# Kernel tuning notes

Measured on AMD Instinct MI355X. Metric: run time of the kernel, lower is better.

Reference implementation:

```python
import jax, jax.numpy as jnp
import numpy as np

B, N, E = 32, 1024, 512   # docs, word-nodes per doc, hyperedges per doc
V = 50001                 # n_node + 1 (padding idx 0)
D = 300                   # initialFeatureSize == n_hid
H = 300                   # hiddenSize (output of gat2)
NEG = -9e15


def _leaky(v, alpha):
    return jnp.where(v > 0, v, alpha * v)


def _hypergat_layer(x, adj, w, w2, w3, a, a2, wc, alpha, concat):
    # x: [B,N,Fin], adj: [B,E,N] 0/1 incidence. Eval mode: dropout = identity.
    Fo = w2.shape[1]
    x4 = x @ w2                                   # [B,N,Fo]
    if w is not None:                             # transfer=True branch
        x = x @ w                                 # [B,N,Fo]
    mask = adj > 0                                # [B,E,N]
    # edge attention: score per node, constant word-context query
    s1 = _leaky(wc @ a[:Fo, 0] + x4 @ a[Fo:, 0], alpha)          # [B,N]
    att_edge = jax.nn.softmax(jnp.where(mask, s1[:, None, :], NEG), axis=2)  # [B,E,N]
    edge = att_edge @ x                           # [B,E,Fo] hyperedge features
    edge4 = edge @ w3                             # [B,E,Fo]
    # node attention: score(node n, edge e) = leaky(x4[n]@a2_top + edge4[e]@a2_bot)
    sc = _leaky((x4 @ a2[:Fo, 0])[:, None, :] + (edge4 @ a2[Fo:, 0])[:, :, None], alpha)  # [B,E,N]
    att_node = jax.nn.softmax(jnp.where(mask, sc, NEG).transpose(0, 2, 1), axis=2)        # [B,N,E]
    node = att_node @ edge                        # [B,N,Fo]
    return jax.nn.elu(node) if concat else node


def setup_inputs() -> dict:
    key = jax.random.key(0)
    ks = jax.random.split(key, 16)
    stdv = 1.0 / np.sqrt(H)  # DocumentGraph.reset_parameters uniform_(-stdv, stdv) on all params
    u = lambda k, shape: jax.random.uniform(k, shape, jnp.float32, -stdv, stdv)
    return dict(
        inputs=jax.random.randint(ks[0], (B, N), 0, V),
        HT=(jax.random.uniform(ks[1], (B, E, N)) < 0.10).astype(jnp.int32),
        emb=u(ks[2], (V, D)),
        w2_1=u(ks[3], (D, D)), w3_1=u(ks[4], (D, D)),
        a_1=u(ks[5], (2 * D, 1)), a2_1=u(ks[6], (2 * D, 1)), wc_1=u(ks[7], (D,)),
        w_2=u(ks[8], (D, H)), w2_2=u(ks[9], (D, H)), w3_2=u(ks[10], (H, H)),
        a_2=u(ks[11], (2 * H, 1)), a2_2=u(ks[12], (2 * H, 1)), wc_2=u(ks[13], (H,)),
    )


def reference(inputs, HT, emb, w2_1, w3_1, a_1, a2_1, wc_1,
              w_2, w2_2, w3_2, a_2, a2_2, wc_2):
    x = emb[inputs]                                # [B,N,D] embedding lookup
    # gat1: transfer=False, concat=True, alpha=0.1
    x = _hypergat_layer(x, HT, None, w2_1, w3_1, a_1, a2_1, wc_1, 0.1, True)
    # gat2: transfer=True, bias=False, concat=False, alpha=0.2
    x = _hypergat_layer(x, HT, w_2, w2_2, w3_2, a_2, a2_2, wc_2, 0.2, False)
    return x
```

## Files before the change

### kernel.cpp

```cpp
#include <hip/hip_runtime.h>
#include <hip/hip_bf16.h>

#define CB 32
#define CN 1024
#define CE 512
#define CD 300
#define EP 320
#define UCAP 320

__global__ void k_embed(const int* __restrict__ idx, const float* __restrict__ emb,
                        float* __restrict__ X) {
    int gid = blockIdx.x * blockDim.x + threadIdx.x;
    const int total = CB * CN * 75;
    if (gid >= total) return;
    int r = gid / 75, c = gid % 75;
    int e = idx[r];
    reinterpret_cast<float4*>(X)[(size_t)r * 75 + c] =
        reinterpret_cast<const float4*>(emb)[(size_t)e * 75 + c];
}

__global__ void k_transpose(const int* __restrict__ HT, unsigned char* __restrict__ HTt) {
    __shared__ int tile[32][33];
    int b = blockIdx.z;
    int e0 = blockIdx.x * 32, n0 = blockIdx.y * 32;
    int tx = threadIdx.x, ty = threadIdx.y;
    for (int i = ty; i < 32; i += 8)
        tile[i][tx] = HT[((size_t)b * CE + e0 + i) * CN + n0 + tx];
    __syncthreads();
    for (int i = ty; i < 32; i += 8)
        HTt[((size_t)b * CN + n0 + i) * CE + e0 + tx] = (unsigned char)(tile[tx][i] > 0 ? 1 : 0);
}

__global__ void k_ebits(const int* __restrict__ HT, unsigned long long* __restrict__ ebits) {
    int gw = (blockIdx.x * blockDim.x + threadIdx.x) >> 6;
    int lane = threadIdx.x & 63;
    const int* hrow = HT + (size_t)gw * CN;
#pragma unroll
    for (int c = 0; c < 16; ++c) {
        unsigned long long bal = __ballot(hrow[(c << 6) + lane] != 0);
        if (lane == 0) ebits[(size_t)gw * 16 + c] = bal;
    }
}

__global__ void k_nbits(const unsigned char* __restrict__ HTt, unsigned long long* __restrict__ nbits) {
    int row = (blockIdx.x * blockDim.x + threadIdx.x) >> 6;
    int lane = threadIdx.x & 63;
    const unsigned char* hrow = HTt + (size_t)row * CE;
#pragma unroll
    for (int c = 0; c < 8; ++c) {
        unsigned long long bal = __ballot(hrow[(c << 6) + lane] != 0);
        if (lane == 0) nbits[(size_t)row * 8 + c] = bal;
    }
}

__global__ void k_prep(const float* __restrict__ w2_1, const float* __restrict__ w3_1,
                       const float* __restrict__ a_1, const float* __restrict__ a2_1,
                       const float* __restrict__ w2_2, const float* __restrict__ w3_2,
                       const float* __restrict__ a_2, const float* __restrict__ a2_2,
                       float* __restrict__ vecs) {
    int which = blockIdx.x;
    int t = threadIdx.x;
    if (t >= CD) return;
    const float* W; const float* v;
    switch (which) {
        case 0:  W = w2_1; v = a_1 + CD;  break;
        case 1:  W = w2_1; v = a2_1;      break;
        case 2:  W = w3_1; v = a2_1 + CD; break;
        case 3:  W = w2_2; v = a_2 + CD;  break;
        case 4:  W = w2_2; v = a2_2;      break;
        default: W = w3_2; v = a2_2 + CD; break;
    }
    float s = 0.f;
    for (int j = 0; j < CD; ++j) s += W[(size_t)t * CD + j] * v[j];
    vecs[which * CD + t] = s;
}

__global__ __launch_bounds__(256) void k_gemm300(const float* __restrict__ A,
                                                 const float* __restrict__ W,
                                                 float* __restrict__ C, int M,
                                                 int lda, int ldc) {
    __shared__ float As[64][20];
    __shared__ float Ws[16][68];
    int tid = threadIdx.x;
    int n0 = blockIdx.x * 64, m0 = blockIdx.y * 64;
    int tx = tid & 15, ty = tid >> 4;
    int la_r = tid >> 2, la_c = (tid & 3) << 2;
    int lw_r = tid >> 4, lw_c = (tid & 15) << 2;
    float acc[4][4] = {};
    for (int k0 = 0; k0 < CD; k0 += 16) {
        {
            int kc = k0 + la_c;
            const float* Ap = A + (size_t)(m0 + la_r) * lda + kc;
            float4 av;
            if (kc + 3 < CD) av = *reinterpret_cast<const float4*>(Ap);
            else {
                av.x = kc     < CD ? Ap[0] : 0.f;
                av.y = kc + 1 < CD ? Ap[1] : 0.f;
                av.z = kc + 2 < CD ? Ap[2] : 0.f;
                av.w = 0.f;
            }
            *reinterpret_cast<float4*>(&As[la_r][la_c]) = av;
        }
        {
            int kr = k0 + lw_r;
            float4 wv = {0.f, 0.f, 0.f, 0.f};
            if (kr < CD) {
                const float* Wp = W + (size_t)kr * CD + n0 + lw_c;
                if (n0 + lw_c + 3 < CD) wv = *reinterpret_cast<const float4*>(Wp);
                else {
                    if (n0 + lw_c     < CD) wv.x = Wp[0];
                    if (n0 + lw_c + 1 < CD) wv.y = Wp[1];
                    if (n0 + lw_c + 2 < CD) wv.z = Wp[2];
                }
            }
            *reinterpret_cast<float4*>(&Ws[lw_r][lw_c]) = wv;
        }
        __syncthreads();
#pragma unroll
        for (int k = 0; k < 16; ++k) {
            float av[4];
#pragma unroll
            for (int i = 0; i < 4; ++i) av[i] = As[ty * 4 + i][k];
            float4 bv = *reinterpret_cast<const float4*>(&Ws[k][tx * 4]);
            float bb[4] = {bv.x, bv.y, bv.z, bv.w};
#pragma unroll
            for (int i = 0; i < 4; ++i)
#pragma unroll
                for (int j = 0; j < 4; ++j) acc[i][j] += av[i] * bb[j];
        }
        __syncthreads();
    }
    for (int i = 0; i < 4; ++i) {
        int m = m0 + ty * 4 + i;
        int n = n0 + tx * 4;
        float* Cp = C + (size_t)m * ldc + n;
        if (n + 3 < CD) {
            float4 v = {acc[i][0], acc[i][1], acc[i][2], acc[i][3]};
            *reinterpret_cast<float4*>(Cp) = v;
        } else {
            for (int j = 0; j < 4; ++j) if (n + j < CD) Cp[j] = acc[i][j];
        }
    }
}

__global__ void k_score(const float* __restrict__ X, const float* __restrict__ av,
                        const float* __restrict__ pv, const float* __restrict__ wc,
                        const float* __restrict__ a_orig,
                        float alpha, float* __restrict__ s1, float* __restrict__ p, int M) {
    int gw = (blockIdx.x * blockDim.x + threadIdx.x) >> 6;
    int lane = threadIdx.x & 63;
    if (gw >= M) return;
    const float* row = X + (size_t)gw * CD;
    float d1 = 0.f, d2 = 0.f, dc = 0.f;
    for (int d = lane; d < CD; d += 64) {
        float x = row[d];
        d1 += x * av[d];
        d2 += x * pv[d];
        dc += wc[d] * a_orig[d];
    }
    for (int o = 32; o; o >>= 1) {
        d1 += __shfl_down(d1, o);
        d2 += __shfl_down(d2, o);
        dc += __shfl_down(dc, o);
    }
    if (lane == 0) {
        float v = dc + d1;
        s1[gw] = v > 0.f ? v : alpha * v;
        p[gw] = d2;
    }
}

__global__ __launch_bounds__(1024) void k_bmax(const float* __restrict__ s1,
                                               float* __restrict__ e1) {
    __shared__ float red[16];
    int b = blockIdx.x, t = threadIdx.x;
    float v = s1[b * CN + t];
    float m = v;
    for (int o = 32; o; o >>= 1) m = fmaxf(m, __shfl_xor(m, o));
    if ((t & 63) == 0) red[t >> 6] = m;
    __syncthreads();
    if (t == 0) {
        float mm = red[0];
        for (int i = 1; i < 16; ++i) mm = fmaxf(mm, red[i]);
        red[0] = mm;
    }
    __syncthreads();
    e1[b * CN + t] = __expf(v - red[0]);
}

__global__ __launch_bounds__(256) void k_edge_agg(const unsigned long long* __restrict__ ebits,
        const float* __restrict__ e1, const float* __restrict__ Xs,
        const float* __restrict__ qvec, float* __restrict__ edge, float* __restrict__ q) {
    int i = blockIdx.x;
    int r = i & 7, t = i >> 3;
    int b = (t >> 7) * 8 + r;
    int j = t & 127;
    int gw = b * CE + (j << 2) + (threadIdx.x >> 6);
    int lane = threadIdx.x & 63;
    const unsigned long long* eb = ebits + (size_t)gw * 16;
    const float* e1b = e1 + b * CN;
    const float* Xb = Xs + (size_t)b * CN * CD;
    float acc[5] = {};
    float den = 0.f;
    bool tail = lane < (CD - 256);
    int any = 0;
#pragma unroll
    for (int c = 0; c < 16; ++c) {
        int n0 = c << 6;
        float wv = e1b[n0 + lane];
        unsigned long long bal = eb[c];
        any |= (bal != 0ull);
        while (bal) {
            int jj = (int)__ffsll(bal) - 1;
            bal &= bal - 1ull;
            float w = __shfl(wv, jj);
            const float* row = Xb + (size_t)(n0 + jj) * CD;
            den += w;
            acc[0] += w * row[lane];
            acc[1] += w * row[lane + 64];
            acc[2] += w * row[lane + 128];
            acc[3] += w * row[lane + 192];
            if (tail) acc[4] += w * row[lane + 256];
        }
    }
    float inv = any ? 1.f / den : 0.f;
    float* erow = edge + (size_t)gw * EP;
    float o0 = acc[0] * inv, o1 = acc[1] * inv, o2 = acc[2] * inv, o3 = acc[3] * inv;
    float o4 = tail ? acc[4] * inv : 0.f;
    erow[lane]       = o0;
    erow[lane + 64]  = o1;
    erow[lane + 128] = o2;
    erow[lane + 192] = o3;
    erow[lane + 256] = o4;
    float d2 = o0 * qvec[lane];
    d2 += o1 * qvec[lane + 64];
    d2 += o2 * qvec[lane + 128];
    d2 += o3 * qvec[lane + 192];
    if (tail) d2 += o4 * qvec[lane + 256];
    for (int o = 32; o; o >>= 1) d2 += __shfl_down(d2, o);
    if (lane == 0) q[gw] = d2;
}

#define ACC16(vv, ww) do { \
    acc[0][0] += (ww).x * (vv).x; acc[0][1] += (ww).x * (vv).y; \
    acc[0][2] += (ww).x * (vv).z; acc[0][3] += (ww).x * (vv).w; \
    acc[1][0] += (ww).y * (vv).x; acc[1][1] += (ww).y * (vv).y; \
    acc[1][2] += (ww).y * (vv).z; acc[1][3] += (ww).y * (vv).w; \
    acc[2][0] += (ww).z * (vv).x; acc[2][1] += (ww).z * (vv).y; \
    acc[2][2] += (ww).z * (vv).z; acc[2][3] += (ww).z * (vv).w; \
    acc[3][0] += (ww).w * (vv).x; acc[3][1] += (ww).w * (vv).y; \
    acc[3][2] += (ww).w * (vv).z; acc[3][3] += (ww).w * (vv).w; \
} while (0)

__global__ __launch_bounds__(320, 8) void k_node_attn(const unsigned long long* __restrict__ nbits,
        const float* __restrict__ p, const float* __restrict__ q,
        const float* __restrict__ edge, float alpha, int do_elu, float* __restrict__ out) {
    __shared__ float4 wsc[4][UCAP];
    __shared__ __align__(8) unsigned short ul[4][UCAP];
    __shared__ int ucnt_s[4], flag_s[4];
    __shared__ float gpn[16], gmx[16], gsc[16];
    __shared__ int gct[16];
    int i0 = blockIdx.x;
    int rr = i0 & 7, tt = i0 >> 3;
    int b = (tt >> 6) * 8 + rr;
    int n0 = (tt & 63) << 4;
    int tid = threadIdx.x, wv = tid >> 6, lane = tid & 63;
    const float* qb = q + b * CE;

    if (wv < 4) {
        float pn[4]; const unsigned long long* nb[4];
#pragma unroll
        for (int k = 0; k < 4; ++k) {
            int n = n0 + 4 * wv + k;
            pn[k] = p[b * CN + n];
            nb[k] = nbits + ((size_t)b * CN + n) * 8;
        }
        float sc[4][8];
        int cnt[4] = {0, 0, 0, 0};
        float mx[4] = {-3.4e38f, -3.4e38f, -3.4e38f, -3.4e38f};
        int ubits = 0;
#pragma unroll
        for (int j = 0; j < 8; ++j) {
            int e = lane + (j << 6);
            float qe = qb[e];
            int many = 0;
#pragma unroll
            for (int k = 0; k < 4; ++k) {
                int m = (int)((nb[k][j] >> lane) & 1ull);
                float v = pn[k] + qe;
                v = v > 0.f ? v : alpha * v;
                v = m ? v : -3.0e38f;
                cnt[k] += m; many |= m;
                mx[k] = fmaxf(mx[k], v);
                sc[k][j] = v;
            }
            ubits |= (many ? 1 : 0) << j;
        }
#pragma unroll
        for (int k = 0; k < 4; ++k) {
            for (int o = 32; o; o >>= 1) {
                mx[k] = fmaxf(mx[k], __shfl_xor(mx[k], o));
                cnt[k] += __shfl_xor(cnt[k], o);
            }
        }
        float scale[4];
#pragma unroll
        for (int k = 0; k < 4; ++k) {
            float s = 0.f;
#pragma unroll
            for (int j = 0; j < 8; ++j) { float w8 = __expf(sc[k][j] - mx[k]); sc[k][j] = w8; s += w8; }
            for (int o = 32; o; o >>= 1) s += __shfl_xor(s, o);
            scale[k] = cnt[k] > 0 ? 1.f / s : 1.f;
        }
        int base = 0;
        unsigned long long lmask = (1ull << lane) - 1ull;
#pragma unroll
        for (int j = 0; j < 8; ++j) {
            unsigned long long bal = __ballot((ubits >> j) & 1);
            if ((ubits >> j) & 1) {
                int off = base + (int)__popcll(bal & lmask);
                if (off < UCAP) {
                    ul[wv][off] = (unsigned short)(lane + (j << 6));
                    wsc[wv][off] = make_float4(sc[0][j] * scale[0], sc[1][j] * scale[1],
                                               sc[2][j] * scale[2], sc[3][j] * scale[3]);
                }
            }
            base += (int)__popcll(bal);
        }
        if (lane == 0) {
            ucnt_s[wv] = base < UCAP ? base : UCAP;
            flag_s[wv] = (cnt[0] == 0) | (cnt[1] == 0) | (cnt[2] == 0) | (cnt[3] == 0) |
                         (base > UCAP);
            gpn[wv*4+0]=pn[0]; gmx[wv*4+0]=mx[0]; gsc[wv*4+0]=scale[0]; gct[wv*4+0]=cnt[0];
            gpn[wv*4+1]=pn[1]; gmx[wv*4+1]=mx[1]; gsc[wv*4+1]=scale[1]; gct[wv*4+1]=cnt[1];
            gpn[wv*4+2]=pn[2]; gmx[wv*4+2]=mx[2]; gsc[wv*4+2]=scale[2]; gct[wv*4+2]=cnt[2];
            gpn[wv*4+3]=pn[3]; gmx[wv*4+3]=mx[3]; gsc[wv*4+3]=scale[3]; gct[wv*4+3]=cnt[3];
        }
    }
    __syncthreads();

    int grp = tid / 80;
    int j4 = tid - grp * 80;
    const float4* eb4 = reinterpret_cast<const float4*>(edge + (size_t)b * CE * EP) + j4;
    int cnt = ucnt_s[grp], bad = flag_s[grp];
    float acc[4][4] = {};
    if (!bad) {
        int i = 0;
        for (; i + 4 <= cnt; i += 4) {
            ushort4 uu = *reinterpret_cast<const ushort4*>(&ul[grp][i]);
            float4 w0 = wsc[grp][i],     w1 = wsc[grp][i + 1];
            float4 w2 = wsc[grp][i + 2], w3 = wsc[grp][i + 3];
            float4 v0 = eb4[(size_t)uu.x * 80], v1 = eb4[(size_t)uu.y * 80];
            float4 v2 = eb4[(size_t)uu.z * 80], v3 = eb4[(size_t)uu.w * 80];
            ACC16(v0, w0); ACC16(v1, w1); ACC16(v2, w2); ACC16(v3, w3);
        }
        for (; i < cnt; ++i) {
            int e = ul[grp][i];
            float4 v = eb4[(size_t)e * 80];
            float4 w = wsc[grp][i];
            ACC16(v, w);
        }
    } else {
        float pnk[4], mxk[4], sck[4]; int ctk[4];
        const unsigned long long* nbr[4];
#pragma unroll
        for (int k = 0; k < 4; ++k) {
            pnk[k] = gpn[grp*4+k]; mxk[k] = gmx[grp*4+k]; sck[k] = gsc[grp*4+k]; ctk[k] = gct[grp*4+k];
            nbr[k] = nbits + ((size_t)b * CN + n0 + grp * 4 + k) * 8;
        }
        for (int e = 0; e < CE; ++e) {
            float4 v = eb4[(size_t)e * 80];
            float qe = qb[e];
#pragma unroll
            for (int k = 0; k < 4; ++k) {
                int m = (int)((nbr[k][e >> 6] >> (e & 63)) & 1ull);
                float vv = pnk[k] + qe; vv = vv > 0.f ? vv : alpha * vv;
                float w = ctk[k] == 0 ? (1.f / CE) : (m ? __expf(vv - mxk[k]) * sck[k] : 0.f);
                acc[k][0] += w * v.x; acc[k][1] += w * v.y; acc[k][2] += w * v.z; acc[k][3] += w * v.w;
            }
        }
    }
    if (j4 < 75) {
#pragma unroll
        for (int ni = 0; ni < 4; ++ni) {
            float4 o = {acc[ni][0], acc[ni][1], acc[ni][2], acc[ni][3]};
            if (do_elu) {
                o.x = o.x > 0.f ? o.x : expm1f(o.x);
                o.y = o.y > 0.f ? o.y : expm1f(o.y);
                o.z = o.z > 0.f ? o.z : expm1f(o.z);
                o.w = o.w > 0.f ? o.w : expm1f(o.w);
            }
            *reinterpret_cast<float4*>(out + ((size_t)b * CN + n0 + grp * 4 + ni) * CD + j4 * 4) = o;
        }
    }
}

extern "C" void kernel_launch(void* const* d_in, const int* in_sizes, int n_in,
                              void* d_out, int out_size, void* d_ws, size_t ws_size,
                              hipStream_t stream) {
    const int*   inputs = (const int*)d_in[0];
    const int*   HT     = (const int*)d_in[1];
    const float* emb    = (const float*)d_in[2];
    const float* w2_1   = (const float*)d_in[3];
    const float* w3_1   = (const float*)d_in[4];
    const float* a_1    = (const float*)d_in[5];
    const float* a2_1   = (const float*)d_in[6];
    const float* wc_1   = (const float*)d_in[7];
    const float* w_2    = (const float*)d_in[8];
    const float* w2_2   = (const float*)d_in[9];
    const float* w3_2   = (const float*)d_in[10];
    const float* a_2    = (const float*)d_in[11];
    const float* a2_2   = (const float*)d_in[12];
    const float* wc_2   = (const float*)d_in[13];

    char* ws = (char*)d_ws;
    float* big0                   = (float*)(ws);
    float* big1                   = (float*)(ws + 39321600);
    float* edge                   = (float*)(ws + 78643200);
    unsigned char* HTt            = (unsigned char*)(ws + 99614720);
    unsigned long long* ebits     = (unsigned long long*)(ws + 116391936);
    unsigned long long* nbits     = (unsigned long long*)(ws + 118489088);
    float* s1                     = (float*)(ws + 120586240);
    float* p                      = (float*)(ws + 120717312);
    float* e1                     = (float*)(ws + 120848384);
    float* qv                     = (float*)(ws + 120979456);
    float* vecs                   = (float*)(ws + 121044992);

    k_embed<<<9600, 256, 0, stream>>>(inputs, emb, big0);
    k_transpose<<<dim3(16, 32, 32), dim3(32, 8), 0, stream>>>(HT, HTt);
    k_ebits<<<4096, 256, 0, stream>>>(HT, ebits);
    k_nbits<<<8192, 256, 0, stream>>>(HTt, nbits);
    k_prep<<<6, 320, 0, stream>>>(w2_1, w3_1, a_1, a2_1, w2_2, w3_2, a_2, a2_2, vecs);

    k_score<<<CB * CN / 4, 256, 0, stream>>>(big0, vecs, vecs + CD, wc_1, a_1, 0.1f, s1, p, CB * CN);
    k_bmax<<<CB, 1024, 0, stream>>>(s1, e1);
    k_edge_agg<<<4096, 256, 0, stream>>>(ebits, e1, big0, vecs + 2 * CD, edge, qv);
    k_node_attn<<<2048, 320, 0, stream>>>(nbits, p, qv, edge, 0.1f, 1, big0);

    k_score<<<CB * CN / 4, 256, 0, stream>>>(big0, vecs + 3 * CD, vecs + 4 * CD, wc_2, a_2, 0.2f, s1, p, CB * CN);
    k_gemm300<<<dim3(5, 512), 256, 0, stream>>>(big0, w_2, big1, CB * CN, CD, CD);
    k_bmax<<<CB, 1024, 0, stream>>>(s1, e1);
    k_edge_agg<<<4096, 256, 0, stream>>>(ebits, e1, big1, vecs + 5 * CD, edge, qv);
    k_node_attn<<<2048, 320, 0, stream>>>(nbits, p, qv, edge, 0.2f, 0, (float*)d_out);
}
```

Measured before the change: 675.1 us.

## Build node bitmasks by bit-transposing edge bitmasks; vectorize edge aggregation loads

```diff
diff --git a/kernel.cpp b/kernel.cpp
--- a/kernel.cpp
+++ b/kernel.cpp
@@ -19,18 +19,6 @@
         reinterpret_cast<const float4*>(emb)[(size_t)e * 75 + c];
 }
 
-__global__ void k_transpose(const int* __restrict__ HT, unsigned char* __restrict__ HTt) {
-    __shared__ int tile[32][33];
-    int b = blockIdx.z;
-    int e0 = blockIdx.x * 32, n0 = blockIdx.y * 32;
-    int tx = threadIdx.x, ty = threadIdx.y;
-    for (int i = ty; i < 32; i += 8)
-        tile[i][tx] = HT[((size_t)b * CE + e0 + i) * CN + n0 + tx];
-    __syncthreads();
-    for (int i = ty; i < 32; i += 8)
-        HTt[((size_t)b * CN + n0 + i) * CE + e0 + tx] = (unsigned char)(tile[tx][i] > 0 ? 1 : 0);
-}
-
 __global__ void k_ebits(const int* __restrict__ HT, unsigned long long* __restrict__ ebits) {
     int gw = (blockIdx.x * blockDim.x + threadIdx.x) >> 6;
     int lane = threadIdx.x & 63;
@@ -42,15 +30,18 @@
     }
 }
 
-__global__ void k_nbits(const unsigned char* __restrict__ HTt, unsigned long long* __restrict__ nbits) {
-    int row = (blockIdx.x * blockDim.x + threadIdx.x) >> 6;
-    int lane = threadIdx.x & 63;
-    const unsigned char* hrow = HTt + (size_t)row * CE;
-#pragma unroll
-    for (int c = 0; c < 8; ++c) {
-        unsigned long long bal = __ballot(hrow[(c << 6) + lane] != 0);
-        if (lane == 0) nbits[(size_t)row * 8 + c] = bal;
-    }
+__global__ __launch_bounds__(512) void k_bitT(const unsigned long long* __restrict__ ebits,
+        unsigned long long* __restrict__ nbits) {
+    __shared__ unsigned long long w[8][64];
+    int b = blockIdx.x >> 4, nc = blockIdx.x & 15;
+    int tid = threadIdx.x, ec = tid >> 6, lane = tid & 63;
+    w[ec][lane] = ebits[((size_t)b * CE + (ec << 6) + lane) * 16 + nc];
+    __syncthreads();
+    unsigned long long out = 0;
+#pragma unroll
+    for (int j = 0; j < 64; ++j)
+        out |= ((w[ec][j] >> lane) & 1ull) << j;
+    nbits[((size_t)b * CN + (nc << 6) + lane) * 8 + ec] = out;
 }
 
 __global__ void k_prep(const float* __restrict__ w2_1, const float* __restrict__ w3_1,
@@ -191,18 +182,15 @@
 __global__ __launch_bounds__(256) void k_edge_agg(const unsigned long long* __restrict__ ebits,
         const float* __restrict__ e1, const float* __restrict__ Xs,
         const float* __restrict__ qvec, float* __restrict__ edge, float* __restrict__ q) {
-    int i = blockIdx.x;
-    int r = i & 7, t = i >> 3;
-    int b = (t >> 7) * 8 + r;
-    int j = t & 127;
-    int gw = b * CE + (j << 2) + (threadIdx.x >> 6);
+    int gw = (blockIdx.x * blockDim.x + threadIdx.x) >> 6;
     int lane = threadIdx.x & 63;
+    int b = gw >> 9;
     const unsigned long long* eb = ebits + (size_t)gw * 16;
     const float* e1b = e1 + b * CN;
-    const float* Xb = Xs + (size_t)b * CN * CD;
-    float acc[5] = {};
+    const float4* Xb4 = reinterpret_cast<const float4*>(Xs + (size_t)b * CN * CD);
+    float4 a0 = {0.f, 0.f, 0.f, 0.f}, a1 = {0.f, 0.f, 0.f, 0.f};
     float den = 0.f;
-    bool tail = lane < (CD - 256);
+    bool tail = lane < 11;
     int any = 0;
 #pragma unroll
     for (int c = 0; c < 16; ++c) {
@@ -211,32 +199,50 @@
         unsigned long long bal = eb[c];
         any |= (bal != 0ull);
         while (bal) {
-            int jj = (int)__ffsll(bal) - 1;
-            bal &= bal - 1ull;
-            float w = __shfl(wv, jj);
-            const float* row = Xb + (size_t)(n0 + jj) * CD;
-            den += w;
-            acc[0] += w * row[lane];
-            acc[1] += w * row[lane + 64];
-            acc[2] += w * row[lane + 128];
-            acc[3] += w * row[lane + 192];
-            if (tail) acc[4] += w * row[lane + 256];
+            int j0 = (int)__ffsll(bal) - 1; bal &= bal - 1ull;
+            float w0 = __shfl(wv, j0);
+            const float4* r0 = Xb4 + (size_t)(n0 + j0) * 75;
+            if (bal) {
+                int j1 = (int)__ffsll(bal) - 1; bal &= bal - 1ull;
+                float w1 = __shfl(wv, j1);
+                const float4* r1 = Xb4 + (size_t)(n0 + j1) * 75;
+                float4 v0a = r0[lane];
+                float4 v1a = r1[lane];
+                float4 v0b, v1b;
+                if (tail) { v0b = r0[64 + lane]; v1b = r1[64 + lane]; }
+                den += w0; den += w1;
+                a0.x += w0 * v0a.x; a0.y += w0 * v0a.y; a0.z += w0 * v0a.z; a0.w += w0 * v0a.w;
+                a0.x += w1 * v1a.x; a0.y += w1 * v1a.y; a0.z += w1 * v1a.z; a0.w += w1 * v1a.w;
+                if (tail) {
+                    a1.x += w0 * v0b.x; a1.y += w0 * v0b.y; a1.z += w0 * v0b.z; a1.w += w0 * v0b.w;
+                    a1.x += w1 * v1b.x; a1.y += w1 * v1b.y; a1.z += w1 * v1b.z; a1.w += w1 * v1b.w;
+                }
+            } else {
+                float4 v0a = r0[lane];
+                float4 v0b;
+                if (tail) v0b = r0[64 + lane];
+                den += w0;
+                a0.x += w0 * v0a.x; a0.y += w0 * v0a.y; a0.z += w0 * v0a.z; a0.w += w0 * v0a.w;
+                if (tail) {
+                    a1.x += w0 * v0b.x; a1.y += w0 * v0b.y; a1.z += w0 * v0b.z; a1.w += w0 * v0b.w;
+                }
+            }
         }
     }
     float inv = any ? 1.f / den : 0.f;
-    float* erow = edge + (size_t)gw * EP;
-    float o0 = acc[0] * inv, o1 = acc[1] * inv, o2 = acc[2] * inv, o3 = acc[3] * inv;
-    float o4 = tail ? acc[4] * inv : 0.f;
-    erow[lane]       = o0;
-    erow[lane + 64]  = o1;
-    erow[lane + 128] = o2;
-    erow[lane + 192] = o3;
-    erow[lane + 256] = o4;
-    float d2 = o0 * qvec[lane];
-    d2 += o1 * qvec[lane + 64];
-    d2 += o2 * qvec[lane + 128];
-    d2 += o3 * qvec[lane + 192];
-    if (tail) d2 += o4 * qvec[lane + 256];
+    float4 o0 = {a0.x * inv, a0.y * inv, a0.z * inv, a0.w * inv};
+    float4 o1 = {a1.x * inv, a1.y * inv, a1.z * inv, a1.w * inv};
+    float4* er4 = reinterpret_cast<float4*>(edge + (size_t)gw * EP);
+    er4[lane] = o0;
+    if (tail) er4[64 + lane] = o1;
+    else if (lane < 16) er4[64 + lane] = make_float4(0.f, 0.f, 0.f, 0.f);
+    const float4* qv4 = reinterpret_cast<const float4*>(qvec);
+    float4 qa = qv4[lane];
+    float d2 = o0.x * qa.x + o0.y * qa.y + o0.z * qa.z + o0.w * qa.w;
+    if (tail) {
+        float4 qb2 = qv4[64 + lane];
+        d2 += o1.x * qb2.x + o1.y * qb2.y + o1.z * qb2.z + o1.w * qb2.w;
+    }
     for (int o = 32; o; o >>= 1) d2 += __shfl_down(d2, o);
     if (lane == 0) q[gw] = d2;
 }
@@ -260,10 +266,8 @@
     __shared__ int ucnt_s[4], flag_s[4];
     __shared__ float gpn[16], gmx[16], gsc[16];
     __shared__ int gct[16];
-    int i0 = blockIdx.x;
-    int rr = i0 & 7, tt = i0 >> 3;
-    int b = (tt >> 6) * 8 + rr;
-    int n0 = (tt & 63) << 4;
+    int blk = blockIdx.x;
+    int b = blk >> 6, n0 = (blk & 63) << 4;
     int tid = threadIdx.x, wv = tid >> 6, lane = tid & 63;
     const float* qb = q + b * CE;
 
@@ -414,22 +418,20 @@
     const float* wc_2   = (const float*)d_in[13];
 
     char* ws = (char*)d_ws;
-    float* big0                   = (float*)(ws);
-    float* big1                   = (float*)(ws + 39321600);
-    float* edge                   = (float*)(ws + 78643200);
-    unsigned char* HTt            = (unsigned char*)(ws + 99614720);
-    unsigned long long* ebits     = (unsigned long long*)(ws + 116391936);
-    unsigned long long* nbits     = (unsigned long long*)(ws + 118489088);
-    float* s1                     = (float*)(ws + 120586240);
-    float* p                      = (float*)(ws + 120717312);
-    float* e1                     = (float*)(ws + 120848384);
-    float* qv                     = (float*)(ws + 120979456);
-    float* vecs                   = (float*)(ws + 121044992);
+    float* big0               = (float*)(ws);
+    float* big1               = (float*)(ws + 39321600);
+    float* edge               = (float*)(ws + 78643200);
+    unsigned long long* ebits = (unsigned long long*)(ws + 99614720);
+    unsigned long long* nbits = (unsigned long long*)(ws + 101711872);
+    float* s1                 = (float*)(ws + 103809024);
+    float* p                  = (float*)(ws + 103940096);
+    float* e1                 = (float*)(ws + 104071168);
+    float* qv                 = (float*)(ws + 104202240);
+    float* vecs               = (float*)(ws + 104267776);
 
     k_embed<<<9600, 256, 0, stream>>>(inputs, emb, big0);
-    k_transpose<<<dim3(16, 32, 32), dim3(32, 8), 0, stream>>>(HT, HTt);
     k_ebits<<<4096, 256, 0, stream>>>(HT, ebits);
-    k_nbits<<<8192, 256, 0, stream>>>(HTt, nbits);
+    k_bitT<<<512, 512, 0, stream>>>(ebits, nbits);
     k_prep<<<6, 320, 0, stream>>>(w2_1, w3_1, a_1, a2_1, w2_2, w3_2, a_2, a2_2, vecs);
 
     k_score<<<CB * CN / 4, 256, 0, stream>>>(big0, vecs, vecs + CD, wc_1, a_1, 0.1f, s1, p, CB * CN);
```

After: 735.4 us. 8.9% more time.
